# Kernel optimization log

Measured on AMD Instinct MI355X. Metric: run time of the kernel, lower is better.

The kernel has to match this reference:

```python
import jax, jax.numpy as jnp
import numpy as np

T, B, D, H = 1024, 8, 1024, 16
NH = D // H  # 64, per-head width (nhid)
W_SCALE = 0.02


def setup_inputs() -> dict:
    key = jax.random.key(0)
    ks = jax.random.split(key, 10)
    return {
        "input_tensor": jax.random.normal(ks[0], (T, B, D), jnp.float32),
        "keys_vector": jax.random.normal(ks[1], (T, B, D), jnp.float32),
        "values_vector": jax.random.normal(ks[2], (T, B, D), jnp.float32),
        # per-head projection weights: [H, D, NH]
        "Wq": jax.random.normal(ks[3], (H, D, NH), jnp.float32) * W_SCALE,
        "bq": jnp.zeros((H, NH), jnp.float32),
        "Wk": jax.random.normal(ks[4], (H, D, NH), jnp.float32) * W_SCALE,
        "bk": jnp.zeros((H, NH), jnp.float32),
        "Wv": jax.random.normal(ks[5], (H, D, NH), jnp.float32) * W_SCALE,
        "bv": jnp.zeros((H, NH), jnp.float32),
        # output projection after concatenating heads
        "Wo": jax.random.normal(ks[6], (D, D), jnp.float32) * W_SCALE,
        "bo": jnp.zeros((D,), jnp.float32),
        "mask": 1,  # True: causal (growing key slice per timestep)
    }


def reference(input_tensor, keys_vector, values_vector, Wq, bq, Wk, bk, Wv, bv, Wo, bo, mask):
    # Vectorized equivalent of the per-timestep loop: query at step t attends
    # to keys/values[:t+1] when mask is set, else to the full sequence.
    q = jnp.einsum('tbd,hdk->tbhk', input_tensor, Wq) + bq   # [T,B,H,NH]
    k = jnp.einsum('sbd,hdk->sbhk', keys_vector, Wk) + bk    # [T,B,H,NH]
    v = jnp.einsum('sbd,hdk->sbhk', values_vector, Wv) + bv  # [T,B,H,NH]

    scale = 1.0 / jnp.sqrt(jnp.float32(NH))
    scores = jnp.einsum('tbhk,sbhk->bhts', q, k) * scale     # [B,H,T,T]
    if mask:
        causal = jnp.tril(jnp.ones((T, T), dtype=bool))      # s <= t
        scores = jnp.where(causal[None, None], scores, jnp.float32(-1e9))
    attn = jax.nn.softmax(scores, axis=-1)                   # over key dim s

    out = jnp.einsum('bhts,sbhk->tbhk', attn, v)             # [T,B,H,NH]
    out = out.reshape(T, B, D)                               # concat heads
    return out @ Wo.T + bo                                   # [T,B,D]
```

## Files before the change

### kernel.cpp

```cpp
#include <hip/hip_runtime.h>

typedef short bf16x8 __attribute__((ext_vector_type(8)));
typedef float f32x4 __attribute__((ext_vector_type(4)));
typedef float f32x16 __attribute__((ext_vector_type(16)));

typedef const __attribute__((address_space(1))) void* gptr_t;
typedef __attribute__((address_space(3))) void* sptr_t;

#define Z16 {0.f,0.f,0.f,0.f,0.f,0.f,0.f,0.f,0.f,0.f,0.f,0.f,0.f,0.f,0.f,0.f}
#define VMCNT(n) asm volatile("s_waitcnt vmcnt(" #n ")" ::: "memory")
#define LGKM0 asm volatile("s_waitcnt lgkmcnt(0)" ::: "memory")
#define SCHEDB __builtin_amdgcn_sched_barrier(0)
#define SBAR __builtin_amdgcn_s_barrier()

__device__ __forceinline__ void glds16(const void* g, void* s) {
  __builtin_amdgcn_global_load_lds((gptr_t)g, (sptr_t)s, 16, 0, 0);
}

__device__ __forceinline__ unsigned short f2bf(float x) {
  unsigned u = __float_as_uint(x);
  u = u + 0x7fffu + ((u >> 16) & 1u);
  return (unsigned short)(u >> 16);
}

__device__ __forceinline__ unsigned packbf(float lo, float hi) {
  return (unsigned)f2bf(lo) | (((unsigned)f2bf(hi)) << 16);
}

__global__ void cvtall(const float* __restrict__ X, const float* __restrict__ KY,
                       const float* __restrict__ VY, const float* __restrict__ Wo,
                       unsigned short* __restrict__ XB, unsigned short* __restrict__ WOB) {
  int stride = gridDim.x * blockDim.x;
  for (int i = blockIdx.x * blockDim.x + threadIdx.x; i < 6553600; i += stride) {
    const float* in; unsigned short* out; int k;
    if (i < 2097152)      { in = X;  out = XB;            k = i; }
    else if (i < 4194304) { in = KY; out = XB + 8388608;  k = i - 2097152; }
    else if (i < 6291456) { in = VY; out = XB + 16777216; k = i - 4194304; }
    else                  { in = Wo; out = WOB;           k = i - 6291456; }
    float4 v = ((const float4*)in)[k];
    uint2 r;
    r.x = packbf(v.x, v.y);
    r.y = packbf(v.z, v.w);
    ((uint2*)out)[k] = r;
  }
}

__global__ __launch_bounds__(256) void wtrans(const float* __restrict__ Wq,
                                              const float* __restrict__ Wk,
                                              const float* __restrict__ Wv,
                                              unsigned short* __restrict__ WT) {
  int m = blockIdx.y >> 4, h = blockIdx.y & 15, d0 = blockIdx.x * 64;
  const float* src = (m == 0 ? Wq : (m == 1 ? Wk : Wv)) + (size_t)h * 65536;
  __shared__ float tile[64][65];
  int c = (threadIdx.x & 15) * 4, r0 = threadIdx.x >> 4;
#pragma unroll
  for (int rr = 0; rr < 4; ++rr) {
    int dr = rr * 16 + r0;
    float4 v = *(const float4*)(src + (size_t)(d0 + dr) * 64 + c);
    tile[dr][c + 0] = v.x; tile[dr][c + 1] = v.y;
    tile[dr][c + 2] = v.z; tile[dr][c + 3] = v.w;
  }
  __syncthreads();
#pragma unroll
  for (int rr = 0; rr < 4; ++rr) {
    int kr = rr * 16 + r0;
    uint2 pk;
    pk.x = packbf(tile[c + 0][kr], tile[c + 1][kr]);
    pk.y = packbf(tile[c + 2][kr], tile[c + 3][kr]);
    *(uint2*)(WT + ((size_t)(m * 1024 + h * 64 + kr)) * 1024 + d0 + c) = pk;
  }
}

template <int MODE>
__global__ __launch_bounds__(512, 2) void gemm256(const unsigned short* __restrict__ Ab,
                                                  const unsigned short* __restrict__ Bb,
                                                  const float* __restrict__ bi0,
                                                  const float* __restrict__ bi1,
                                                  const float* __restrict__ bi2,
                                                  void* __restrict__ outp) {
  extern __shared__ __align__(16) char lds[];
  const int K = 1024;
  int z = blockIdx.z;
  const unsigned short* A = Ab + (size_t)z * 8192 * 1024;
  const unsigned short* BT = Bb + (size_t)z * 1024 * 1024;
  const float* bias = (MODE == 0) ? (z == 0 ? bi0 : (z == 1 ? bi1 : bi2)) : bi0;
  int m0 = blockIdx.x * 256, n0 = blockIdx.y * 128;
  int tid = threadIdx.x, wid = tid >> 6, l = tid & 63;
  int ml5 = l & 31, hi1 = l >> 5;
  int wr = (wid & 3) * 64, wc = (wid >> 2) * 64;
  int srow = l >> 3;
  int ksw = ((l & 7) << 4) ^ ((srow & 7) << 4);
  f32x16 acc[2][2] = {};
#pragma unroll
  for (int t0 = 0; t0 < 2; ++t0) {
    char* nb = lds + t0 * 49152;
    int ko = t0 * 64;
#pragma unroll
    for (int i = 0; i < 4; ++i) {
      int c = wid * 4 + i;
      glds16((const char*)(A + (size_t)(m0 + c * 8 + srow) * K + ko) + ksw, nb + c * 1024);
    }
#pragma unroll
    for (int i = 0; i < 2; ++i) {
      int c2 = wid * 2 + i;
      glds16((const char*)(BT + (size_t)(n0 + c2 * 8 + srow) * K + ko) + ksw, nb + 32768 + c2 * 1024);
    }
  }
  int bsel = 0;
  for (int t = 0; t < 16; ++t) {
    SCHEDB; LGKM0;
    if (t < 15) { VMCNT(6); } else { VMCNT(0); }
    SBAR; SCHEDB;
    if (t + 2 < 16) {
      int b2 = bsel + 2; if (b2 >= 3) b2 -= 3;
      char* nb = lds + b2 * 49152;
      int ko = (t + 2) * 64;
#pragma unroll
      for (int i = 0; i < 4; ++i) {
        int c = wid * 4 + i;
        glds16((const char*)(A + (size_t)(m0 + c * 8 + srow) * K + ko) + ksw, nb + c * 1024);
      }
#pragma unroll
      for (int i = 0; i < 2; ++i) {
        int c2 = wid * 2 + i;
        glds16((const char*)(BT + (size_t)(n0 + c2 * 8 + srow) * K + ko) + ksw, nb + 32768 + c2 * 1024);
      }
    }
    char* As = lds + bsel * 49152;
    char* Bs = As + 32768;
#pragma unroll
    for (int ks = 0; ks < 4; ++ks) {
      int koff = ks * 32 + hi1 * 16;
      int ra0 = wr + ml5, ra1 = wr + 32 + ml5;
      int rb0 = wc + ml5, rb1 = wc + 32 + ml5;
      bf16x8 a0 = *(const bf16x8*)(As + ra0 * 128 + (koff ^ ((ra0 & 7) << 4)));
      bf16x8 a1 = *(const bf16x8*)(As + ra1 * 128 + (koff ^ ((ra1 & 7) << 4)));
      bf16x8 b0 = *(const bf16x8*)(Bs + rb0 * 128 + (koff ^ ((rb0 & 7) << 4)));
      bf16x8 b1 = *(const bf16x8*)(Bs + rb1 * 128 + (koff ^ ((rb1 & 7) << 4)));
      __builtin_amdgcn_s_setprio(1);
      acc[0][0] = __builtin_amdgcn_mfma_f32_32x32x16_bf16(a0, b0, acc[0][0], 0, 0, 0);
      acc[0][1] = __builtin_amdgcn_mfma_f32_32x32x16_bf16(a0, b1, acc[0][1], 0, 0, 0);
      acc[1][0] = __builtin_amdgcn_mfma_f32_32x32x16_bf16(a1, b0, acc[1][0], 0, 0, 0);
      acc[1][1] = __builtin_amdgcn_mfma_f32_32x32x16_bf16(a1, b1, acc[1][1], 0, 0, 0);
      __builtin_amdgcn_s_setprio(0);
    }
    bsel += 1; if (bsel >= 3) bsel = 0;
  }
  __syncthreads();
  if (MODE == 1) {
#pragma unroll
    for (int nf = 0; nf < 2; ++nf) {
      int col = wc + nf * 32 + ml5;
      float bv = bias[n0 + col];
#pragma unroll
      for (int mf = 0; mf < 2; ++mf)
#pragma unroll
        for (int r = 0; r < 16; ++r) {
          int row = wr + mf * 32 + (r & 3) + 8 * (r >> 2) + 4 * hi1;
          int byte = col * 4;
          *(float*)(lds + row * 512 + ((byte & ~15) ^ ((row & 7) << 4)) + (byte & 15)) =
              acc[mf][nf][r] + bv;
        }
    }
    __syncthreads();
    int rr = tid >> 1, q = tid & 1;
    float* drow = (float*)outp + (size_t)(m0 + rr) * 1024 + n0 + q * 64;
#pragma unroll
    for (int j = 0; j < 16; ++j) {
      uint4 d = *(uint4*)(lds + rr * 512 + ((q * 256 + j * 16) ^ ((rr & 7) << 4)));
      *(uint4*)(drow + j * 4) = d;
    }
    return;
  }
#pragma unroll
  for (int nf = 0; nf < 2; ++nf) {
    int col = wc + nf * 32 + ml5;
    float bv = bias[n0 + col];
#pragma unroll
    for (int mf = 0; mf < 2; ++mf)
#pragma unroll
      for (int r = 0; r < 16; ++r) {
        int row = wr + mf * 32 + (r & 3) + 8 * (r >> 2) + 4 * hi1;
        float v = acc[mf][nf][r] + bv;
        float pv = __shfl_xor(v, 1);
        unsigned pk = (ml5 & 1) ? packbf(pv, v) : packbf(v, pv);
        *(unsigned*)(lds + row * 256 + (((col * 2) & ~3) ^ ((row & 7) << 4))) = pk;
      }
  }
  __syncthreads();
  unsigned short* ob = (unsigned short*)outp + (size_t)z * 8388608;
  if (z != 2) {
    int rr = tid >> 1, hh = tid & 1;
    int t = (m0 + rr) >> 3, b = (m0 + rr) & 7;
    int h = (n0 >> 6) + hh;
    unsigned short* dst = ob + (size_t)(b * 16 + h) * 65536 + (size_t)t * 64;
#pragma unroll
    for (int j = 0; j < 8; ++j) {
      uint4 d = *(uint4*)(lds + rr * 256 + ((hh * 128 + j * 16) ^ ((rr & 7) << 4)));
      *(uint4*)(dst + j * 8) = d;
    }
  } else {
    int t0 = m0 >> 3;
#pragma unroll
    for (int q = 0; q < 2; ++q) {
      int id = q * 512 + tid;
      int k = id & 63;
      int bh2 = id >> 6;
      int b = bh2 >> 1, hh = bh2 & 1;
      int colb = (hh * 64 + k) * 2;
      union { unsigned short u[32]; uint4 v[4]; } tmp;
#pragma unroll
      for (int tp = 0; tp < 32; ++tp)
        tmp.u[tp] = *(unsigned short*)(lds + (tp * 8 + b) * 256 + (colb ^ (b << 4)));
      int h = (n0 >> 6) + hh;
      unsigned short* dst = ob + (size_t)(b * 16 + h) * 65536 + (size_t)k * 1024 + t0;
#pragma unroll
      for (int j = 0; j < 4; ++j) *(uint4*)(dst + j * 8) = tmp.v[j];
    }
  }
}

__global__ __launch_bounds__(512, 4) void attn_k(const unsigned short* __restrict__ Qp,
                                                 const unsigned short* __restrict__ Kp,
                                                 const unsigned short* __restrict__ VTp,
                                                 unsigned short* __restrict__ Op,
                                                 const int* __restrict__ maskp) {
  int lin = blockIdx.x;
  int xcd = lin & 7, idx = lin >> 3;
  int bh = xcd + 8 * (idx >> 2);
  int j = idx & 3;
  const size_t base = (size_t)bh * 65536;
  int tid = threadIdx.x, w = tid >> 6, l = tid & 63;
  int ml5 = l & 31, hi1 = l >> 5;
  int half = w & 1, pi = w >> 1;
  int stripe = (pi == 0) ? j : (pi == 1) ? (15 - j) : (pi == 2) ? (7 - j) : (8 + j);
  int tw0 = stripe * 64 + half * 32;
  int t_glob = tw0 + ml5;
  __shared__ __align__(16) char lds[32768];
  int msk = *maskp;
  const float CE = 0.18033688011112042f;
  bf16x8 bq[4];
#pragma unroll
  for (int kd = 0; kd < 4; ++kd)
    bq[kd] = *(const bf16x8*)(Qp + base + (size_t)t_glob * 64 + kd * 16 + hi1 * 8);
  f32x16 o0 = Z16, o1 = Z16;
  float m_run = -3e38f, l_run = 0.f;
  int nt = msk ? (16 - j) : 16;
  int diag = stripe;
  int srow = l >> 3, kphys = (l & 7) << 4;
  int row = w * 8 + srow;
  int klog = kphys ^ (srow << 4);
  int swz = (ml5 & 7) << 4;
  glds16((const char*)(Kp + base + (size_t)row * 64) + klog, lds + w * 1024);
  glds16((const char*)(VTp + base + (size_t)row * 1024) + klog, lds + 8192 + w * 1024);
  int cur = 0;
  for (int st = 0; st < nt; ++st) {
    if (st + 1 < nt) {
      char* nb = lds + (cur ^ 1) * 16384;
      glds16((const char*)(Kp + base + (size_t)((st + 1) * 64 + row) * 64) + klog, nb + w * 1024);
      glds16((const char*)(VTp + base + (size_t)row * 1024 + (st + 1) * 64) + klog, nb + 8192 + w * 1024);
      VMCNT(4);
    } else {
      VMCNT(0);
    }
    SCHEDB; SBAR; SCHEDB;
    if (!msk || st <= diag) {
      char* Ks = lds + cur * 16384;
      char* Vs = Ks + 8192;
      f32x16 s0 = Z16, s1 = Z16;
      __builtin_amdgcn_s_setprio(1);
#pragma unroll
      for (int kd = 0; kd < 4; ++kd) {
        int koff = kd * 32 + hi1 * 16;
        bf16x8 a0 = *(const bf16x8*)(Ks + ml5 * 128 + (koff ^ swz));
        bf16x8 a1 = *(const bf16x8*)(Ks + (32 + ml5) * 128 + (koff ^ swz));
        s0 = __builtin_amdgcn_mfma_f32_32x32x16_bf16(a0, bq[kd], s0, 0, 0, 0);
        s1 = __builtin_amdgcn_mfma_f32_32x32x16_bf16(a1, bq[kd], s1, 0, 0, 0);
      }
      __builtin_amdgcn_s_setprio(0);
      if (msk && st == diag) {
#pragma unroll
        for (int r = 0; r < 16; ++r) {
          int sl = st * 64 + (r & 3) + 8 * (r >> 2) + 4 * hi1;
          if (sl > t_glob) s0[r] = -1e30f;
          if (sl + 32 > t_glob) s1[r] = -1e30f;
        }
      }
      float t8[8];
#pragma unroll
      for (int r = 0; r < 8; ++r)
        t8[r] = fmaxf(fmaxf(s0[r], s0[r + 8]), fmaxf(s1[r], s1[r + 8]));
      float tm = fmaxf(fmaxf(fmaxf(t8[0], t8[1]), fmaxf(t8[2], t8[3])),
                       fmaxf(fmaxf(t8[4], t8[5]), fmaxf(t8[6], t8[7])));
      tm = fmaxf(tm, __shfl_xor(tm, 32));
      float m_old = m_run;
      float m_new = fmaxf(m_old, tm);
      m_run = m_new;
      float sc2 = exp2f((m_old - m_new) * CE);
      float mC = m_new * CE;
#pragma unroll
      for (int r = 0; r < 16; ++r) {
        s0[r] = exp2f(fmaf(s0[r], CE, -mC));
        s1[r] = exp2f(fmaf(s1[r], CE, -mC));
      }
      float a8[8];
#pragma unroll
      for (int r = 0; r < 8; ++r)
        a8[r] = (s0[r] + s0[r + 8]) + (s1[r] + s1[r + 8]);
      float ps = ((a8[0] + a8[1]) + (a8[2] + a8[3])) + ((a8[4] + a8[5]) + (a8[6] + a8[7]));
      ps += __shfl_xor(ps, 32);
      l_run = l_run * sc2 + ps;
#pragma unroll
      for (int r = 0; r < 16; ++r) { o0[r] *= sc2; o1[r] *= sc2; }
      unsigned cc0[4][2], cc1[4][2];
#pragma unroll
      for (int q = 0; q < 4; ++q) {
        cc0[q][0] = packbf(s0[4 * q + 0], s0[4 * q + 1]);
        cc0[q][1] = packbf(s0[4 * q + 2], s0[4 * q + 3]);
        cc1[q][0] = packbf(s1[4 * q + 0], s1[4 * q + 1]);
        cc1[q][1] = packbf(s1[4 * q + 2], s1[4 * q + 3]);
      }
#define CCa(a, p) ((a) < 4 ? cc0[(a) & 3][p] : cc1[(a) & 3][p])
      union U4 { unsigned u[4]; bf16x8 v; };
      bf16x8 pb[4];
#pragma unroll
      for (int kb = 0; kb < 4; ++kb) {
        U4 t;
#pragma unroll
        for (int p = 0; p < 2; ++p) {
          unsigned x = CCa(2 * kb, p), y = CCa(2 * kb + 1, p);
          unsigned v = hi1 ? x : y;
          unsigned wv = hi1 ? y : x;
          unsigned vs = __shfl_xor(v, 32);
          t.u[p]     = hi1 ? vs : wv;
          t.u[2 + p] = hi1 ? wv : vs;
        }
        pb[kb] = t.v;
      }
#undef CCa
      __builtin_amdgcn_s_setprio(1);
#pragma unroll
      for (int kb = 0; kb < 4; ++kb) {
        int koff = kb * 32 + hi1 * 16;
        bf16x8 v0 = *(const bf16x8*)(Vs + ml5 * 128 + (koff ^ swz));
        bf16x8 v1 = *(const bf16x8*)(Vs + (32 + ml5) * 128 + (koff ^ swz));
        o0 = __builtin_amdgcn_mfma_f32_32x32x16_bf16(v0, pb[kb], o0, 0, 0, 0);
        o1 = __builtin_amdgcn_mfma_f32_32x32x16_bf16(v1, pb[kb], o1, 0, 0, 0);
      }
      __builtin_amdgcn_s_setprio(0);
    }
    SCHEDB; LGKM0; SBAR;
    cur ^= 1;
  }
  float rl = 1.0f / l_run;
  int b = bh >> 4, h = bh & 15;
  unsigned short* orow = Op + (size_t)(t_glob * 8 + b) * 1024 + h * 64;
#pragma unroll
  for (int q2 = 0; q2 < 4; ++q2) {
    uint2 pk0, pk1;
    pk0.x = packbf(o0[4 * q2 + 0] * rl, o0[4 * q2 + 1] * rl);
    pk0.y = packbf(o0[4 * q2 + 2] * rl, o0[4 * q2 + 3] * rl);
    *(uint2*)(orow + 4 * hi1 + 8 * q2) = pk0;
    pk1.x = packbf(o1[4 * q2 + 0] * rl, o1[4 * q2 + 1] * rl);
    pk1.y = packbf(o1[4 * q2 + 2] * rl, o1[4 * q2 + 3] * rl);
    *(uint2*)(orow + 32 + 4 * hi1 + 8 * q2) = pk1;
  }
}

extern "C" void kernel_launch(void* const* d_in, const int* in_sizes, int n_in,
                              void* d_out, int out_size, void* d_ws, size_t ws_size,
                              hipStream_t stream) {
  const float* X  = (const float*)d_in[0];
  const float* KY = (const float*)d_in[1];
  const float* VY = (const float*)d_in[2];
  const float* Wq = (const float*)d_in[3];
  const float* bq = (const float*)d_in[4];
  const float* Wk = (const float*)d_in[5];
  const float* bk = (const float*)d_in[6];
  const float* Wv = (const float*)d_in[7];
  const float* bv = (const float*)d_in[8];
  const float* Wo = (const float*)d_in[9];
  const float* bo = (const float*)d_in[10];
  const int* mask = (const int*)d_in[11];
  char* ws = (char*)d_ws;
  unsigned short* XB  = (unsigned short*)(ws);
  unsigned short* WT  = (unsigned short*)(ws + 48ll * 1024 * 1024);
  unsigned short* WOB = (unsigned short*)(ws + 54ll * 1024 * 1024);
  unsigned short* QP  = (unsigned short*)(ws + 56ll * 1024 * 1024);
  unsigned short* OP  = (unsigned short*)(ws + 104ll * 1024 * 1024);

  cvtall<<<2048, 256, 0, stream>>>(X, KY, VY, Wo, XB, WOB);
  wtrans<<<dim3(16, 48), 256, 0, stream>>>(Wq, Wk, Wv, WT);
  gemm256<0><<<dim3(32, 8, 3), 512, 147456, stream>>>(XB, WT, bq, bk, bv, QP);
  attn_k<<<512, 512, 0, stream>>>(QP, QP + 8388608, QP + 16777216, OP, mask);
  gemm256<1><<<dim3(32, 8, 1), 512, 147456, stream>>>(OP, WOB, bo, bo, bo, d_out);
}
```

Baseline: 210.2 us.

## Switch GEMM to 16x16x32 MFMA with two-phase interleaved load/compute schedule

Replaces the 32x32x16 MFMA tiling with 16x16x32 MFMA over a 4x4 fragment grid per wave, and splits each K-tile into two halves. Global-to-LDS prefetch issues are spread across the two halves, and barriers sit around each MFMA cluster, so loads overlap compute in a ping-pong style. This is meant to hide LDS and global latency better. The cost is more barriers and a different register footprint.

```diff
diff --git a/kernel.cpp b/kernel.cpp
--- a/kernel.cpp
+++ b/kernel.cpp
@@ -85,78 +85,99 @@
   const unsigned short* BT = Bb + (size_t)z * 1024 * 1024;
   const float* bias = (MODE == 0) ? (z == 0 ? bi0 : (z == 1 ? bi1 : bi2)) : bi0;
   int m0 = blockIdx.x * 256, n0 = blockIdx.y * 128;
-  int tid = threadIdx.x, wid = tid >> 6, l = tid & 63;
-  int ml5 = l & 31, hi1 = l >> 5;
+  int tid = threadIdx.x, wid = tid >> 6, l = tid & 63, ml = l & 15, hi = l >> 4;
   int wr = (wid & 3) * 64, wc = (wid >> 2) * 64;
   int srow = l >> 3;
-  int ksw = ((l & 7) << 4) ^ ((srow & 7) << 4);
-  f32x16 acc[2][2] = {};
-#pragma unroll
-  for (int t0 = 0; t0 < 2; ++t0) {
-    char* nb = lds + t0 * 49152;
-    int ko = t0 * 64;
-#pragma unroll
-    for (int i = 0; i < 4; ++i) {
-      int c = wid * 4 + i;
-      glds16((const char*)(A + (size_t)(m0 + c * 8 + srow) * K + ko) + ksw, nb + c * 1024);
-    }
-#pragma unroll
-    for (int i = 0; i < 2; ++i) {
-      int c2 = wid * 2 + i;
-      glds16((const char*)(BT + (size_t)(n0 + c2 * 8 + srow) * K + ko) + ksw, nb + 32768 + c2 * 1024);
-    }
-  }
+  int ksw = ((l & 7) << 4) ^ (srow << 4);
+  f32x4 acc[4][4] = {};
+#define STG_A(i, buf, ko)                                                          \
+  { int c = wid * 4 + (i);                                                         \
+    glds16((const char*)(A + (size_t)(m0 + c * 8 + srow) * K + (ko)) + ksw,        \
+           (buf) + c * 1024); }
+#define STG_B(i, buf, ko)                                                          \
+  { int c2 = wid * 2 + (i);                                                        \
+    glds16((const char*)(BT + (size_t)(n0 + c2 * 8 + srow) * K + (ko)) + ksw,      \
+           (buf) + 32768 + c2 * 1024); }
+  STG_A(0, lds, 0); STG_A(1, lds, 0); STG_A(2, lds, 0); STG_A(3, lds, 0);
+  STG_B(0, lds, 0); STG_B(1, lds, 0);
+  {
+    char* b1 = lds + 49152;
+    STG_A(0, b1, 64); STG_A(1, b1, 64); STG_A(2, b1, 64); STG_A(3, b1, 64);
+    STG_B(0, b1, 64); STG_B(1, b1, 64);
+  }
+  VMCNT(6);
+  SCHEDB; SBAR; SCHEDB;
   int bsel = 0;
   for (int t = 0; t < 16; ++t) {
-    SCHEDB; LGKM0;
-    if (t < 15) { VMCNT(6); } else { VMCNT(0); }
-    SBAR; SCHEDB;
-    if (t + 2 < 16) {
-      int b2 = bsel + 2; if (b2 >= 3) b2 -= 3;
-      char* nb = lds + b2 * 49152;
-      int ko = (t + 2) * 64;
-#pragma unroll
-      for (int i = 0; i < 4; ++i) {
-        int c = wid * 4 + i;
-        glds16((const char*)(A + (size_t)(m0 + c * 8 + srow) * K + ko) + ksw, nb + c * 1024);
-      }
-#pragma unroll
-      for (int i = 0; i < 2; ++i) {
-        int c2 = wid * 2 + i;
-        glds16((const char*)(BT + (size_t)(n0 + c2 * 8 + srow) * K + ko) + ksw, nb + 32768 + c2 * 1024);
-      }
-    }
     char* As = lds + bsel * 49152;
     char* Bs = As + 32768;
-#pragma unroll
-    for (int ks = 0; ks < 4; ++ks) {
-      int koff = ks * 32 + hi1 * 16;
-      int ra0 = wr + ml5, ra1 = wr + 32 + ml5;
-      int rb0 = wc + ml5, rb1 = wc + 32 + ml5;
-      bf16x8 a0 = *(const bf16x8*)(As + ra0 * 128 + (koff ^ ((ra0 & 7) << 4)));
-      bf16x8 a1 = *(const bf16x8*)(As + ra1 * 128 + (koff ^ ((ra1 & 7) << 4)));
-      bf16x8 b0 = *(const bf16x8*)(Bs + rb0 * 128 + (koff ^ ((rb0 & 7) << 4)));
-      bf16x8 b1 = *(const bf16x8*)(Bs + rb1 * 128 + (koff ^ ((rb1 & 7) << 4)));
+    int b2 = bsel + 2; if (b2 >= 3) b2 -= 3;
+    char* nb = lds + b2 * 49152;
+    int ko2 = (t + 2) * 64;
+    bool st = (t + 2 < 16);
+    {
+      bf16x8 af[4], bfr[4];
+#pragma unroll
+      for (int mf = 0; mf < 4; ++mf) {
+        int row = wr + mf * 16 + ml;
+        af[mf] = *(const bf16x8*)(As + row * 128 + ((hi << 4) ^ ((row & 7) << 4)));
+      }
+#pragma unroll
+      for (int nf = 0; nf < 4; ++nf) {
+        int row = wc + nf * 16 + ml;
+        bfr[nf] = *(const bf16x8*)(Bs + row * 128 + ((hi << 4) ^ ((row & 7) << 4)));
+      }
+      if (st) { STG_A(0, nb, ko2); STG_A(1, nb, ko2); STG_A(2, nb, ko2); }
+      SCHEDB; SBAR; LGKM0; SCHEDB;
       __builtin_amdgcn_s_setprio(1);
-      acc[0][0] = __builtin_amdgcn_mfma_f32_32x32x16_bf16(a0, b0, acc[0][0], 0, 0, 0);
-      acc[0][1] = __builtin_amdgcn_mfma_f32_32x32x16_bf16(a0, b1, acc[0][1], 0, 0, 0);
-      acc[1][0] = __builtin_amdgcn_mfma_f32_32x32x16_bf16(a1, b0, acc[1][0], 0, 0, 0);
-      acc[1][1] = __builtin_amdgcn_mfma_f32_32x32x16_bf16(a1, b1, acc[1][1], 0, 0, 0);
+#pragma unroll
+      for (int mf = 0; mf < 4; ++mf)
+#pragma unroll
+        for (int nf = 0; nf < 4; ++nf)
+          acc[mf][nf] = __builtin_amdgcn_mfma_f32_16x16x32_bf16(af[mf], bfr[nf], acc[mf][nf], 0, 0, 0);
       __builtin_amdgcn_s_setprio(0);
+      SCHEDB; SBAR;
+    }
+    {
+      bf16x8 af[4], bfr[4];
+#pragma unroll
+      for (int mf = 0; mf < 4; ++mf) {
+        int row = wr + mf * 16 + ml;
+        af[mf] = *(const bf16x8*)(As + row * 128 + ((64 + (hi << 4)) ^ ((row & 7) << 4)));
+      }
+#pragma unroll
+      for (int nf = 0; nf < 4; ++nf) {
+        int row = wc + nf * 16 + ml;
+        bfr[nf] = *(const bf16x8*)(Bs + row * 128 + ((64 + (hi << 4)) ^ ((row & 7) << 4)));
+      }
+      if (st) { STG_A(3, nb, ko2); STG_B(0, nb, ko2); STG_B(1, nb, ko2); }
+      if (t < 14) { VMCNT(6); }
+      else if (t == 14) { VMCNT(0); }
+      SCHEDB; SBAR; LGKM0; SCHEDB;
+      __builtin_amdgcn_s_setprio(1);
+#pragma unroll
+      for (int mf = 0; mf < 4; ++mf)
+#pragma unroll
+        for (int nf = 0; nf < 4; ++nf)
+          acc[mf][nf] = __builtin_amdgcn_mfma_f32_16x16x32_bf16(af[mf], bfr[nf], acc[mf][nf], 0, 0, 0);
+      __builtin_amdgcn_s_setprio(0);
+      SCHEDB; SBAR;
     }
     bsel += 1; if (bsel >= 3) bsel = 0;
   }
+#undef STG_A
+#undef STG_B
   __syncthreads();
   if (MODE == 1) {
 #pragma unroll
-    for (int nf = 0; nf < 2; ++nf) {
-      int col = wc + nf * 32 + ml5;
+    for (int nf = 0; nf < 4; ++nf) {
+      int col = wc + nf * 16 + ml;
       float bv = bias[n0 + col];
 #pragma unroll
-      for (int mf = 0; mf < 2; ++mf)
-#pragma unroll
-        for (int r = 0; r < 16; ++r) {
-          int row = wr + mf * 32 + (r & 3) + 8 * (r >> 2) + 4 * hi1;
+      for (int mf = 0; mf < 4; ++mf)
+#pragma unroll
+        for (int r = 0; r < 4; ++r) {
+          int row = wr + mf * 16 + (hi << 2) + r;
           int byte = col * 4;
           *(float*)(lds + row * 512 + ((byte & ~15) ^ ((row & 7) << 4)) + (byte & 15)) =
               acc[mf][nf][r] + bv;
@@ -173,17 +194,17 @@
     return;
   }
 #pragma unroll
-  for (int nf = 0; nf < 2; ++nf) {
-    int col = wc + nf * 32 + ml5;
+  for (int nf = 0; nf < 4; ++nf) {
+    int col = wc + nf * 16 + ml;
     float bv = bias[n0 + col];
 #pragma unroll
-    for (int mf = 0; mf < 2; ++mf)
-#pragma unroll
-      for (int r = 0; r < 16; ++r) {
-        int row = wr + mf * 32 + (r & 3) + 8 * (r >> 2) + 4 * hi1;
+    for (int mf = 0; mf < 4; ++mf)
+#pragma unroll
+      for (int r = 0; r < 4; ++r) {
+        int row = wr + mf * 16 + (hi << 2) + r;
         float v = acc[mf][nf][r] + bv;
         float pv = __shfl_xor(v, 1);
-        unsigned pk = (ml5 & 1) ? packbf(pv, v) : packbf(v, pv);
+        unsigned pk = (ml & 1) ? packbf(pv, v) : packbf(v, pv);
         *(unsigned*)(lds + row * 256 + (((col * 2) & ~3) ^ ((row & 7) << 4))) = pk;
       }
   }
```

Result: faster. 204.4 us (-2.7%).
